# Optimization experiments

Hardware: AMD Instinct MI355X
Metric: run time of the kernel (lower is better)

Reference implementation:

```python
import math
import jax, jax.numpy as jnp
import numpy as np

IMAGE_SIZE = 224


def _resize_bilinear(img, out_h, out_w):
    """PyTorch F.interpolate(mode='bilinear', align_corners=False) equivalent.
    img: [B, H, W] -> [B, out_h, out_w]. No antialiasing (matches torch default)."""
    B, H, W = img.shape

    def coords(out, size):
        r = jnp.maximum((jnp.arange(out, dtype=jnp.float32) + 0.5) * (size / out) - 0.5, 0.0)
        i0 = jnp.minimum(jnp.floor(r).astype(jnp.int32), size - 1)
        i1 = jnp.minimum(i0 + 1, size - 1)
        w = r - i0.astype(jnp.float32)
        return i0, i1, w

    r0, r1, wr = coords(out_h, H)
    c0, c1, wc = coords(out_w, W)
    rows = img[:, r0, :] * (1.0 - wr)[None, :, None] + img[:, r1, :] * wr[None, :, None]
    out = rows[:, :, c0] * (1.0 - wc)[None, None, :] + rows[:, :, c1] * wc[None, None, :]
    return out


def _normalize_minmax(x, eps=1e-8):
    mn = x.min()
    mx = x.max()
    return jnp.where(mx - mn < eps, jnp.zeros_like(x), (x - mn) / (mx - mn + eps))


def _grid_embed(vals, n):
    """Row-major scatter of vals[:, :n] into a ceil(sqrt(n))^2 grid (zero padded)."""
    B = vals.shape[0]
    gs = int(math.ceil(math.sqrt(n)))
    pad = gs * gs - n
    return jnp.pad(vals, ((0, 0), (0, pad))).reshape(B, gs, gs)


def setup_inputs() -> dict:
    key = jax.random.key(0)
    hidden_state = jax.random.normal(key, (32, 512, 4096, 1), dtype=jnp.float32)
    return {"hidden_state": hidden_state}


def reference(hidden_state):
    B, E, N, _ = hidden_state.shape
    x = hidden_state[..., 0]  # [B, E, N]

    # temporal view: mean over nodes -> [B, E] -> grid -> resize
    t_grid = _grid_embed(x.mean(axis=2), E)
    temporal = _normalize_minmax(_resize_bilinear(t_grid, IMAGE_SIZE, IMAGE_SIZE))

    # spatial view: mean over embedding dim -> [B, N] -> grid -> resize
    s_grid = _grid_embed(x.mean(axis=1), N)
    spatial = _normalize_minmax(_resize_bilinear(s_grid, IMAGE_SIZE, IMAGE_SIZE))

    # correlation view: row-normalized centered features, [B, E, E] correlation
    xc = x - x.mean(axis=2, keepdims=True)
    xn = xc / (jnp.linalg.norm(xc, axis=2, keepdims=True) + 1e-8)
    corr = jnp.einsum('bin,bjn->bij', xn, xn)  # [B, E, E]
    correlation = _normalize_minmax(_resize_bilinear(corr, IMAGE_SIZE, IMAGE_SIZE))

    # [B, 3, image_size, image_size]
    return jnp.stack([temporal, spatial, correlation], axis=1)
```

## Files before the change

### kernel.cpp

```cpp
#include <hip/hip_runtime.h>
#include <hip/hip_bf16.h>
#include <math.h>

#define IMG 224
#define PIX (IMG*IMG)
#define B_ 32
#define E_ 512
#define N_ 4096
#define SV_BLOCKS 256
#define SC_ ((float)(512.0/224.0))
#define RPB 16
#define NCHUNK 32
#define KSPLIT 2
#define KLEN (N_/KSPLIT)
#define NTILE 10

typedef __attribute__((ext_vector_type(8))) short bf16x8;
typedef __attribute__((ext_vector_type(4))) float f32x4;

__device__ inline unsigned short f2bf(float f){
  unsigned u = __float_as_uint(f);
  unsigned r = (u + 0x7FFFu + ((u >> 16) & 1u)) >> 16;
  return (unsigned short)r;
}

__global__ void __launch_bounds__(256) stats_y(const float* __restrict__ x,
                                               float* __restrict__ meanv,
                                               float* __restrict__ colpart,
                                               ushort* __restrict__ y){
  int b = blockIdx.x >> 5, chunk = blockIdx.x & 31;
  int e0 = chunk << 4;
  int t = threadIdx.x;
  __shared__ short sInv[512];
  __shared__ float sW[224];
  __shared__ float red[2][16];
  sInv[t] = -1; sInv[t + 256] = -1;
  __syncthreads();
  if (t < 224){
    float r = fmaxf(((float)t + 0.5f) * SC_ - 0.5f, 0.f);
    int r0 = min((int)r, E_ - 1);
    sW[t] = r - (float)r0;
    sInv[r0] = (short)t;
  }
  __syncthreads();

  float cur[16], prev[16], nxt[16], csum[16];
  #pragma unroll
  for (int j = 0; j < 16; j++){ csum[j] = 0.f; prev[j] = 0.f; }
  const float4* row0 = (const float4*)(x + ((size_t)b * E_ + e0) * N_);
  #pragma unroll
  for (int k = 0; k < 4; k++) *(float4*)(cur + 4 * k) = row0[t + 256 * k];
  float pmu = 0.f, prn = 0.f;

  for (int idx = 0; idx <= RPB; idx++){
    int e = e0 + idx;
    if (e >= E_) break;
    bool hasNext = (idx < RPB) && (e + 1 < E_);
    if (hasNext){
      const float4* nr = (const float4*)(x + ((size_t)b * E_ + e + 1) * N_);
      #pragma unroll
      for (int k = 0; k < 4; k++) *(float4*)(nxt + 4 * k) = nr[t + 256 * k];
    }
    float s = 0.f, ss = 0.f;
    #pragma unroll
    for (int j = 0; j < 16; j++){ s += cur[j]; ss += cur[j] * cur[j]; }
    #pragma unroll
    for (int o = 32; o; o >>= 1){ s += __shfl_down(s, o); ss += __shfl_down(ss, o); }
    int wv = t >> 6, ln = t & 63, p = idx & 1;
    if (ln == 0){ red[p][wv] = s; red[p][8 + wv] = ss; }
    __syncthreads();
    float S  = red[p][0] + red[p][1] + red[p][2] + red[p][3];
    float SS = red[p][8] + red[p][9] + red[p][10] + red[p][11];
    float mu = S * (1.f / N_);
    float var = fmaxf(SS - S * S * (1.f / N_), 0.f);
    float rn = 1.f / (sqrtf(var) + 1e-8f);
    if (idx < RPB){
      #pragma unroll
      for (int j = 0; j < 16; j++) csum[j] += cur[j];
      if (t == 0) meanv[b * E_ + e] = mu;
    }
    if (idx >= 1){
      int i = sInv[e - 1];
      if (i >= 0){
        float w = sW[i];
        float a0 = (1.f - w) * prn, a1 = w * rn;
        float cc = -(a0 * pmu + a1 * mu);
        ushort* yo = y + ((size_t)b * IMG + i) * N_;
        #pragma unroll
        for (int k = 0; k < 4; k++){
          union { ushort u[4]; int2 v; } pk;
          #pragma unroll
          for (int j = 0; j < 4; j++)
            pk.u[j] = f2bf(a0 * prev[4*k+j] + a1 * cur[4*k+j] + cc);
          *(int2*)(yo + 1024 * k + 4 * t) = pk.v;
        }
      }
    }
    pmu = mu; prn = rn;
    #pragma unroll
    for (int j = 0; j < 16; j++){ prev[j] = cur[j]; if (hasNext) cur[j] = nxt[j]; }
  }
  float* cp = colpart + ((size_t)(b * NCHUNK + chunk)) * N_;
  #pragma unroll
  for (int k = 0; k < 4; k++) *(float4*)(cp + 1024 * k + 4 * t) = *(float4*)(csum + 4 * k);
}

__global__ void __launch_bounds__(256) col_finalize(const float* __restrict__ colpart,
                                                    float* __restrict__ colmean){
  int b = blockIdx.x >> 4;
  int n = ((blockIdx.x & 15) << 8) + threadIdx.x;
  float s = 0.f;
  #pragma unroll
  for (int c = 0; c < NCHUNK; c++) s += colpart[((size_t)(b * NCHUNK + c)) * N_ + n];
  colmean[b * N_ + n] = s * (1.f / E_);
}

__device__ inline float grid_val(const float* v, int gs, int n, int r, int c){
  int idx = r * gs + c;
  return (idx < n) ? v[idx] : 0.f;
}
__device__ inline float bilin(const float* v, int gs, int n, int i, int j){
  float sc = (float)((double)gs / 224.0);
  float r = fmaxf(((float)i + 0.5f) * sc - 0.5f, 0.f);
  float c = fmaxf(((float)j + 0.5f) * sc - 0.5f, 0.f);
  int r0 = min((int)r, gs - 1), c0 = min((int)c, gs - 1);
  int r1 = min(r0 + 1, gs - 1), c1 = min(c0 + 1, gs - 1);
  float wr = r - (float)r0, wc = c - (float)c0;
  float v00 = grid_val(v, gs, n, r0, c0), v10 = grid_val(v, gs, n, r1, c0);
  float v01 = grid_val(v, gs, n, r0, c1), v11 = grid_val(v, gs, n, r1, c1);
  float ra = v00 * (1.f - wr) + v10 * wr;
  float rb = v01 * (1.f - wr) + v11 * wr;
  return ra * (1.f - wc) + rb * wc;
}

__global__ void __launch_bounds__(256) sv_minmax(const float* __restrict__ meanv,
                                                 const float* __restrict__ colmean,
                                                 float* __restrict__ scr){
  float tmn = INFINITY, tmx = -INFINITY, smn = INFINITY, smx = -INFINITY;
  for (int g = blockIdx.x * 256 + threadIdx.x; g < B_ * PIX; g += SV_BLOCKS * 256){
    int b = g / PIX, p = g - b * PIX;
    int i = p / IMG, j = p - i * IMG;
    float tv = bilin(meanv   + b * E_, 23, E_, i, j);
    float sv = bilin(colmean + b * N_, 64, N_, i, j);
    tmn = fminf(tmn, tv); tmx = fmaxf(tmx, tv);
    smn = fminf(smn, sv); smx = fmaxf(smx, sv);
  }
  #pragma unroll
  for (int o = 32; o; o >>= 1){
    tmn = fminf(tmn, __shfl_down(tmn, o)); tmx = fmaxf(tmx, __shfl_down(tmx, o));
    smn = fminf(smn, __shfl_down(smn, o)); smx = fmaxf(smx, __shfl_down(smx, o));
  }
  __shared__ float red[4][4];
  int wv = threadIdx.x >> 6, ln = threadIdx.x & 63;
  if (ln == 0){ red[wv][0] = tmn; red[wv][1] = tmx; red[wv][2] = smn; red[wv][3] = smx; }
  __syncthreads();
  if (threadIdx.x == 0){
    scr[blockIdx.x * 4 + 0] = fminf(fminf(red[0][0], red[1][0]), fminf(red[2][0], red[3][0]));
    scr[blockIdx.x * 4 + 1] = fmaxf(fmaxf(red[0][1], red[1][1]), fmaxf(red[2][1], red[3][1]));
    scr[blockIdx.x * 4 + 2] = fminf(fminf(red[0][2], red[1][2]), fminf(red[2][2], red[3][2]));
    scr[blockIdx.x * 4 + 3] = fmaxf(fmaxf(red[0][3], red[1][3]), fmaxf(red[2][3], red[3][3]));
  }
}

#define LDSTR 72
__device__ const int TI_[NTILE] = {0,0,0,0,1,1,1,2,2,3};
__device__ const int TJ_[NTILE] = {0,1,2,3,1,2,3,2,3,3};

__global__ void __launch_bounds__(256) corr_gemm_sk(const ushort* __restrict__ y,
                                                    float* __restrict__ partials){
  int xcd  = blockIdx.x & 7;
  int slot = blockIdx.x >> 3;
  int b    = (xcd << 2) + (slot / 20);
  int rem  = slot % 20;
  int ks   = rem / 10;
  int tile = rem - ks * 10;
  int bt   = b * NTILE + tile;
  int ti = TI_[tile], tj = TJ_[tile];
  const ushort* yb = y + (size_t)b * IMG * N_ + (size_t)ks * KLEN;
  __shared__ ushort lA[64 * LDSTR];
  __shared__ ushort lB[64 * LDSTR];
  int t = threadIdx.x;
  int wv = t >> 6, ln = t & 63;
  int wm = wv & 1, wn = wv >> 1;
  int quad = ln >> 4, l16 = ln & 15;
  f32x4 acc[2][2] = {};
  int s = t & 7, r2 = t >> 3;
  int rA0 = min(ti * 64 + r2,      223), rA1 = min(ti * 64 + r2 + 32, 223);
  int rB0 = min(tj * 64 + r2,      223), rB1 = min(tj * 64 + r2 + 32, 223);
  for (int k0 = 0; k0 < KLEN; k0 += 64){
    int4 a0 = *(const int4*)(yb + (size_t)rA0 * N_ + k0 + s * 8);
    int4 a1 = *(const int4*)(yb + (size_t)rA1 * N_ + k0 + s * 8);
    int4 b0v = *(const int4*)(yb + (size_t)rB0 * N_ + k0 + s * 8);
    int4 b1v = *(const int4*)(yb + (size_t)rB1 * N_ + k0 + s * 8);
    __syncthreads();
    *(int4*)(lA + r2 * LDSTR + s * 8)        = a0;
    *(int4*)(lA + (r2 + 32) * LDSTR + s * 8) = a1;
    *(int4*)(lB + r2 * LDSTR + s * 8)        = b0v;
    *(int4*)(lB + (r2 + 32) * LDSTR + s * 8) = b1v;
    __syncthreads();
    #pragma unroll
    for (int kk = 0; kk < 2; kk++){
      bf16x8 af0 = *(const bf16x8*)(lA + (wm * 32 + l16)      * LDSTR + kk * 32 + quad * 8);
      bf16x8 af1 = *(const bf16x8*)(lA + (wm * 32 + 16 + l16) * LDSTR + kk * 32 + quad * 8);
      bf16x8 bf0 = *(const bf16x8*)(lB + (wn * 32 + l16)      * LDSTR + kk * 32 + quad * 8);
      bf16x8 bf1 = *(const bf16x8*)(lB + (wn * 32 + 16 + l16) * LDSTR + kk * 32 + quad * 8);
      acc[0][0] = __builtin_amdgcn_mfma_f32_16x16x32_bf16(af0, bf0, acc[0][0], 0, 0, 0);
      acc[0][1] = __builtin_amdgcn_mfma_f32_16x16x32_bf16(af0, bf1, acc[0][1], 0, 0, 0);
      acc[1][0] = __builtin_amdgcn_mfma_f32_16x16x32_bf16(af1, bf0, acc[1][0], 0, 0, 0);
      acc[1][1] = __builtin_amdgcn_mfma_f32_16x16x32_bf16(af1, bf1, acc[1][1], 0, 0, 0);
    }
  }
  float* pp = partials + ((size_t)ks * (B_ * NTILE) + bt) * 4096 + t * 16;
  #pragma unroll
  for (int im = 0; im < 2; im++)
    #pragma unroll
    for (int in = 0; in < 2; in++)
      *(f32x4*)(pp + 4 * (im * 2 + in)) = acc[im][in];
}

__global__ void __launch_bounds__(256) corr_reduce(const float* __restrict__ partials,
                                                   float* __restrict__ out,
                                                   float* __restrict__ scr){
  int bt = blockIdx.x;
  int b = bt / NTILE, tile = bt - b * NTILE;
  int ti = TI_[tile], tj = TJ_[tile];
  bool diag = (ti == tj);
  int t = threadIdx.x;
  int wv = t >> 6, ln = t & 63;
  int wm = wv & 1, wn = wv >> 1;
  int quad = ln >> 4, l16 = ln & 15;
  f32x4 acc[2][2];
  #pragma unroll
  for (int im = 0; im < 2; im++)
    #pragma unroll
    for (int in = 0; in < 2; in++){
      f32x4 a = {0.f, 0.f, 0.f, 0.f};
      #pragma unroll
      for (int ks = 0; ks < KSPLIT; ks++)
        a += *(const f32x4*)(partials + ((size_t)ks * (B_ * NTILE) + bt) * 4096
                             + t * 16 + 4 * (im * 2 + in));
      acc[im][in] = a;
    }
  float mn = INFINITY, mx = -INFINITY;
  float* ov = out + ((size_t)b * 3 + 2) * PIX;
  #pragma unroll
  for (int im = 0; im < 2; im++)
    #pragma unroll
    for (int in = 0; in < 2; in++){
      int gi0 = ti * 64 + wm * 32 + im * 16 + quad * 4;
      int gj  = tj * 64 + wn * 32 + in * 16 + l16;
      #pragma unroll
      for (int rg = 0; rg < 4; rg++){
        int gi = gi0 + rg;
        if (gi < IMG && gj < IMG){
          float v = acc[im][in][rg];
          ov[gi * IMG + gj] = v;
          mn = fminf(mn, v); mx = fmaxf(mx, v);
        }
      }
      if (!diag && gj < IMG && gi0 < IMG){
        float4 tv;
        tv.x = acc[im][in][0]; tv.y = acc[im][in][1];
        tv.z = acc[im][in][2]; tv.w = acc[im][in][3];
        *(float4*)(ov + gj * IMG + gi0) = tv;
      }
    }
  #pragma unroll
  for (int o = 32; o; o >>= 1){
    mn = fminf(mn, __shfl_down(mn, o)); mx = fmaxf(mx, __shfl_down(mx, o));
  }
  __shared__ float red[4][2];
  if (ln == 0){ red[wv][0] = mn; red[wv][1] = mx; }
  __syncthreads();
  if (t == 0){
    scr[bt * 2 + 0] = fminf(fminf(red[0][0], red[1][0]), fminf(red[2][0], red[3][0]));
    scr[bt * 2 + 1] = fmaxf(fmaxf(red[0][1], red[1][1]), fmaxf(red[2][1], red[3][1]));
  }
}

__global__ void __launch_bounds__(256) reduce_slots(const float* __restrict__ sv_scr,
                                                    const float* __restrict__ corr_scr,
                                                    float* __restrict__ slots){
  int t = threadIdx.x;
  float tmn = sv_scr[4*t+0], tmx = sv_scr[4*t+1];
  float smn = sv_scr[4*t+2], smx = sv_scr[4*t+3];
  float cmn = INFINITY, cmx = -INFINITY;
  for (int idx = t; idx < B_ * NTILE; idx += 256){
    cmn = fminf(cmn, corr_scr[2*idx]);
    cmx = fmaxf(cmx, corr_scr[2*idx+1]);
  }
  #pragma unroll
  for (int o = 32; o; o >>= 1){
    tmn = fminf(tmn, __shfl_down(tmn, o)); tmx = fmaxf(tmx, __shfl_down(tmx, o));
    smn = fminf(smn, __shfl_down(smn, o)); smx = fmaxf(smx, __shfl_down(smx, o));
    cmn = fminf(cmn, __shfl_down(cmn, o)); cmx = fmaxf(cmx, __shfl_down(cmx, o));
  }
  __shared__ float red[4][6];
  int wv = t >> 6, ln = t & 63;
  if (ln == 0){
    red[wv][0]=tmn; red[wv][1]=tmx; red[wv][2]=smn;
    red[wv][3]=smx; red[wv][4]=cmn; red[wv][5]=cmx;
  }
  __syncthreads();
  if (t == 0){
    slots[0] = fminf(fminf(red[0][0],red[1][0]), fminf(red[2][0],red[3][0]));
    slots[1] = fmaxf(fmaxf(red[0][1],red[1][1]), fmaxf(red[2][1],red[3][1]));
    slots[2] = fminf(fminf(red[0][2],red[1][2]), fminf(red[2][2],red[3][2]));
    slots[3] = fmaxf(fmaxf(red[0][3],red[1][3]), fmaxf(red[2][3],red[3][3]));
    slots[4] = fminf(fminf(red[0][4],red[1][4]), fminf(red[2][4],red[3][4]));
    slots[5] = fmaxf(fmaxf(red[0][5],red[1][5]), fmaxf(red[2][5],red[3][5]));
  }
}

__global__ void __launch_bounds__(256) final_write(const float* __restrict__ meanv,
                                                   const float* __restrict__ colmean,
                                                   float* __restrict__ out,
                                                   const float* __restrict__ slots){
  int g = blockIdx.x * 256 + threadIdx.x;
  float tmn = slots[0], tmx = slots[1];
  float smn = slots[2], smx = slots[3];
  int b = g / PIX, p = g - b * PIX;
  int i = p / IMG, j = p - i * IMG;
  float tv = bilin(meanv   + b * E_, 23, E_, i, j);
  float sv = bilin(colmean + b * N_, 64, N_, i, j);
  float td = tmx - tmn, sd = smx - smn;
  out[((size_t)b * 3 + 0) * PIX + p] = (td < 1e-8f) ? 0.f : (tv - tmn) / (td + 1e-8f);
  out[((size_t)b * 3 + 1) * PIX + p] = (sd < 1e-8f) ? 0.f : (sv - smn) / (sd + 1e-8f);
  if (g < B_ * PIX / 4){
    float cmn = slots[4], cmx = slots[5];
    float cd = cmx - cmn;
    float inv = 1.f / (cd + 1e-8f);
    bool z = cd < 1e-8f;
    int c = g * 4;
    int bb = c / PIX, pp = c - bb * PIX;
    float* oc = out + ((size_t)bb * 3 + 2) * PIX + pp;
    float4 v = *(float4*)oc;
    v.x = z ? 0.f : (v.x - cmn) * inv;
    v.y = z ? 0.f : (v.y - cmn) * inv;
    v.z = z ? 0.f : (v.z - cmn) * inv;
    v.w = z ? 0.f : (v.w - cmn) * inv;
    *(float4*)oc = v;
  }
}

extern "C" void kernel_launch(void* const* d_in, const int* in_sizes, int n_in,
                              void* d_out, int out_size, void* d_ws, size_t ws_size,
                              hipStream_t stream){
  const float* x = (const float*)d_in[0];
  float* out = (float*)d_out;
  char* ws = (char*)d_ws;
  float* slots    = (float*)(ws + 0);
  float* meanv    = (float*)(ws + 256);
  float* colmean  = meanv + B_ * E_;
  float* colpart  = colmean + B_ * N_;
  float* sv_scr   = colpart + (size_t)B_ * NCHUNK * N_;
  float* corr_scr = sv_scr + SV_BLOCKS * 4;
  size_t y_off = ((size_t)((char*)(corr_scr + B_ * NTILE * 2) - ws) + 255) & ~(size_t)255;
  ushort* y = (ushort*)(ws + y_off);
  size_t p_off = (y_off + (size_t)B_ * IMG * N_ * 2 + 255) & ~(size_t)255;
  float* partials = (float*)(ws + p_off);

  hipLaunchKernelGGL(stats_y, dim3(B_ * NCHUNK), dim3(256), 0, stream,
                     x, meanv, colpart, y);
  hipLaunchKernelGGL(corr_gemm_sk, dim3(KSPLIT * B_ * NTILE), dim3(256), 0, stream,
                     y, partials);
  hipLaunchKernelGGL(corr_reduce, dim3(B_ * NTILE), dim3(256), 0, stream,
                     partials, out, corr_scr);
  hipLaunchKernelGGL(col_finalize, dim3(B_ * 16), dim3(256), 0, stream,
                     colpart, colmean);
  hipLaunchKernelGGL(sv_minmax, dim3(SV_BLOCKS), dim3(256), 0, stream,
                     meanv, colmean, sv_scr);
  hipLaunchKernelGGL(reduce_slots, dim3(1), dim3(256), 0, stream,
                     sv_scr, corr_scr, slots);
  hipLaunchKernelGGL(final_write, dim3(B_ * PIX / 256), dim3(256), 0, stream,
                     meanv, colmean, out, slots);
}
```

Baseline: 445.3 us.

## Merge small kernels into horizontally fused launches to cut launch count

Cuts the launch chain from seven kernels to four. Column finalization now runs as extra blocks inside the GEMM launch. The correlation reduce and spatial/temporal min-max run as block ranges of one launch. Each final_write block redoes the global slot reduction instead of using a separate single-block kernel. This removes launch overhead and serial gaps between tiny kernels, at the cost of redundant per-block slot reduction work and mixed block types sharing resources.

```diff
diff --git a/kernel.cpp b/kernel.cpp
--- a/kernel.cpp
+++ b/kernel.cpp
@@ -7,13 +7,13 @@
 #define B_ 32
 #define E_ 512
 #define N_ 4096
-#define SV_BLOCKS 256
 #define SC_ ((float)(512.0/224.0))
 #define RPB 16
 #define NCHUNK 32
 #define KSPLIT 2
 #define KLEN (N_/KSPLIT)
 #define NTILE 10
+#define LDSTR 72
 
 typedef __attribute__((ext_vector_type(8))) short bf16x8;
 typedef __attribute__((ext_vector_type(4))) float f32x4;
@@ -105,16 +105,6 @@
   for (int k = 0; k < 4; k++) *(float4*)(cp + 1024 * k + 4 * t) = *(float4*)(csum + 4 * k);
 }
 
-__global__ void __launch_bounds__(256) col_finalize(const float* __restrict__ colpart,
-                                                    float* __restrict__ colmean){
-  int b = blockIdx.x >> 4;
-  int n = ((blockIdx.x & 15) << 8) + threadIdx.x;
-  float s = 0.f;
-  #pragma unroll
-  for (int c = 0; c < NCHUNK; c++) s += colpart[((size_t)(b * NCHUNK + c)) * N_ + n];
-  colmean[b * N_ + n] = s * (1.f / E_);
-}
-
 __device__ inline float grid_val(const float* v, int gs, int n, int r, int c){
   int idx = r * gs + c;
   return (idx < n) ? v[idx] : 0.f;
@@ -133,43 +123,28 @@
   return ra * (1.f - wc) + rb * wc;
 }
 
-__global__ void __launch_bounds__(256) sv_minmax(const float* __restrict__ meanv,
-                                                 const float* __restrict__ colmean,
-                                                 float* __restrict__ scr){
-  float tmn = INFINITY, tmx = -INFINITY, smn = INFINITY, smx = -INFINITY;
-  for (int g = blockIdx.x * 256 + threadIdx.x; g < B_ * PIX; g += SV_BLOCKS * 256){
-    int b = g / PIX, p = g - b * PIX;
-    int i = p / IMG, j = p - i * IMG;
-    float tv = bilin(meanv   + b * E_, 23, E_, i, j);
-    float sv = bilin(colmean + b * N_, 64, N_, i, j);
-    tmn = fminf(tmn, tv); tmx = fmaxf(tmx, tv);
-    smn = fminf(smn, sv); smx = fmaxf(smx, sv);
-  }
-  #pragma unroll
-  for (int o = 32; o; o >>= 1){
-    tmn = fminf(tmn, __shfl_down(tmn, o)); tmx = fmaxf(tmx, __shfl_down(tmx, o));
-    smn = fminf(smn, __shfl_down(smn, o)); smx = fmaxf(smx, __shfl_down(smx, o));
-  }
-  __shared__ float red[4][4];
-  int wv = threadIdx.x >> 6, ln = threadIdx.x & 63;
-  if (ln == 0){ red[wv][0] = tmn; red[wv][1] = tmx; red[wv][2] = smn; red[wv][3] = smx; }
-  __syncthreads();
-  if (threadIdx.x == 0){
-    scr[blockIdx.x * 4 + 0] = fminf(fminf(red[0][0], red[1][0]), fminf(red[2][0], red[3][0]));
-    scr[blockIdx.x * 4 + 1] = fmaxf(fmaxf(red[0][1], red[1][1]), fmaxf(red[2][1], red[3][1]));
-    scr[blockIdx.x * 4 + 2] = fminf(fminf(red[0][2], red[1][2]), fminf(red[2][2], red[3][2]));
-    scr[blockIdx.x * 4 + 3] = fmaxf(fmaxf(red[0][3], red[1][3]), fmaxf(red[2][3], red[3][3]));
-  }
-}
-
-#define LDSTR 72
 __device__ const int TI_[NTILE] = {0,0,0,0,1,1,1,2,2,3};
 __device__ const int TJ_[NTILE] = {0,1,2,3,1,2,3,2,3,3};
 
-__global__ void __launch_bounds__(256) corr_gemm_sk(const ushort* __restrict__ y,
-                                                    float* __restrict__ partials){
-  int xcd  = blockIdx.x & 7;
-  int slot = blockIdx.x >> 3;
+__global__ void __launch_bounds__(256) gemm_colfin(const ushort* __restrict__ y,
+                                                   float* __restrict__ partials,
+                                                   const float* __restrict__ colpart,
+                                                   float* __restrict__ colmean){
+  int bid = blockIdx.x;
+  int t = threadIdx.x;
+  if (bid >= 640){
+    for (int u = bid - 640; u < 512; u += 128){
+      int b = u >> 4;
+      int n = ((u & 15) << 8) + t;
+      float s = 0.f;
+      #pragma unroll
+      for (int c = 0; c < NCHUNK; c++) s += colpart[((size_t)(b * NCHUNK + c)) * N_ + n];
+      colmean[b * N_ + n] = s * (1.f / E_);
+    }
+    return;
+  }
+  int xcd  = bid & 7;
+  int slot = bid >> 3;
   int b    = (xcd << 2) + (slot / 20);
   int rem  = slot % 20;
   int ks   = rem / 10;
@@ -179,7 +154,6 @@
   const ushort* yb = y + (size_t)b * IMG * N_ + (size_t)ks * KLEN;
   __shared__ ushort lA[64 * LDSTR];
   __shared__ ushort lB[64 * LDSTR];
-  int t = threadIdx.x;
   int wv = t >> 6, ln = t & 63;
   int wm = wv & 1, wn = wv >> 1;
   int quad = ln >> 4, l16 = ln & 15;
@@ -218,107 +192,139 @@
       *(f32x4*)(pp + 4 * (im * 2 + in)) = acc[im][in];
 }
 
-__global__ void __launch_bounds__(256) corr_reduce(const float* __restrict__ partials,
-                                                   float* __restrict__ out,
-                                                   float* __restrict__ scr){
-  int bt = blockIdx.x;
-  int b = bt / NTILE, tile = bt - b * NTILE;
-  int ti = TI_[tile], tj = TJ_[tile];
-  bool diag = (ti == tj);
+__global__ void __launch_bounds__(256) reduce_sv(const float* __restrict__ partials,
+                                                 const float* __restrict__ meanv,
+                                                 const float* __restrict__ colmean,
+                                                 float* __restrict__ out,
+                                                 float* __restrict__ corr_scr,
+                                                 float* __restrict__ sv_scr){
+  int bid = blockIdx.x;
   int t = threadIdx.x;
   int wv = t >> 6, ln = t & 63;
-  int wm = wv & 1, wn = wv >> 1;
-  int quad = ln >> 4, l16 = ln & 15;
-  f32x4 acc[2][2];
-  #pragma unroll
-  for (int im = 0; im < 2; im++)
-    #pragma unroll
-    for (int in = 0; in < 2; in++){
-      f32x4 a = {0.f, 0.f, 0.f, 0.f};
-      #pragma unroll
-      for (int ks = 0; ks < KSPLIT; ks++)
-        a += *(const f32x4*)(partials + ((size_t)ks * (B_ * NTILE) + bt) * 4096
-                             + t * 16 + 4 * (im * 2 + in));
-      acc[im][in] = a;
-    }
-  float mn = INFINITY, mx = -INFINITY;
-  float* ov = out + ((size_t)b * 3 + 2) * PIX;
-  #pragma unroll
-  for (int im = 0; im < 2; im++)
-    #pragma unroll
-    for (int in = 0; in < 2; in++){
-      int gi0 = ti * 64 + wm * 32 + im * 16 + quad * 4;
-      int gj  = tj * 64 + wn * 32 + in * 16 + l16;
-      #pragma unroll
-      for (int rg = 0; rg < 4; rg++){
-        int gi = gi0 + rg;
-        if (gi < IMG && gj < IMG){
-          float v = acc[im][in][rg];
-          ov[gi * IMG + gj] = v;
-          mn = fminf(mn, v); mx = fmaxf(mx, v);
+  __shared__ float red[4][4];
+  if (bid < B_ * NTILE){
+    int bt = bid;
+    int b = bt / NTILE, tile = bt - b * NTILE;
+    int ti = TI_[tile], tj = TJ_[tile];
+    bool diag = (ti == tj);
+    int wm = wv & 1, wn = wv >> 1;
+    int quad = ln >> 4, l16 = ln & 15;
+    f32x4 acc[2][2];
+    #pragma unroll
+    for (int im = 0; im < 2; im++)
+      #pragma unroll
+      for (int in = 0; in < 2; in++){
+        f32x4 a = {0.f, 0.f, 0.f, 0.f};
+        #pragma unroll
+        for (int ks = 0; ks < KSPLIT; ks++)
+          a += *(const f32x4*)(partials + ((size_t)ks * (B_ * NTILE) + bt) * 4096
+                               + t * 16 + 4 * (im * 2 + in));
+        acc[im][in] = a;
+      }
+    float mn = INFINITY, mx = -INFINITY;
+    float* ov = out + ((size_t)b * 3 + 2) * PIX;
+    #pragma unroll
+    for (int im = 0; im < 2; im++)
+      #pragma unroll
+      for (int in = 0; in < 2; in++){
+        int gi0 = ti * 64 + wm * 32 + im * 16 + quad * 4;
+        int gj  = tj * 64 + wn * 32 + in * 16 + l16;
+        #pragma unroll
+        for (int rg = 0; rg < 4; rg++){
+          int gi = gi0 + rg;
+          if (gi < IMG && gj < IMG){
+            float v = acc[im][in][rg];
+            ov[gi * IMG + gj] = v;
+            mn = fminf(mn, v); mx = fmaxf(mx, v);
+          }
+        }
+        if (!diag && gj < IMG && gi0 < IMG){
+          float4 tv;
+          tv.x = acc[im][in][0]; tv.y = acc[im][in][1];
+          tv.z = acc[im][in][2]; tv.w = acc[im][in][3];
+          *(float4*)(ov + gj * IMG + gi0) = tv;
         }
       }
-      if (!diag && gj < IMG && gi0 < IMG){
-        float4 tv;
-        tv.x = acc[im][in][0]; tv.y = acc[im][in][1];
-        tv.z = acc[im][in][2]; tv.w = acc[im][in][3];
-        *(float4*)(ov + gj * IMG + gi0) = tv;
-      }
-    }
-  #pragma unroll
-  for (int o = 32; o; o >>= 1){
-    mn = fminf(mn, __shfl_down(mn, o)); mx = fmaxf(mx, __shfl_down(mx, o));
-  }
-  __shared__ float red[4][2];
-  if (ln == 0){ red[wv][0] = mn; red[wv][1] = mx; }
-  __syncthreads();
-  if (t == 0){
-    scr[bt * 2 + 0] = fminf(fminf(red[0][0], red[1][0]), fminf(red[2][0], red[3][0]));
-    scr[bt * 2 + 1] = fmaxf(fmaxf(red[0][1], red[1][1]), fmaxf(red[2][1], red[3][1]));
-  }
-}
-
-__global__ void __launch_bounds__(256) reduce_slots(const float* __restrict__ sv_scr,
-                                                    const float* __restrict__ corr_scr,
-                                                    float* __restrict__ slots){
-  int t = threadIdx.x;
-  float tmn = sv_scr[4*t+0], tmx = sv_scr[4*t+1];
-  float smn = sv_scr[4*t+2], smx = sv_scr[4*t+3];
-  float cmn = INFINITY, cmx = -INFINITY;
-  for (int idx = t; idx < B_ * NTILE; idx += 256){
-    cmn = fminf(cmn, corr_scr[2*idx]);
-    cmx = fmaxf(cmx, corr_scr[2*idx+1]);
-  }
-  #pragma unroll
-  for (int o = 32; o; o >>= 1){
-    tmn = fminf(tmn, __shfl_down(tmn, o)); tmx = fmaxf(tmx, __shfl_down(tmx, o));
-    smn = fminf(smn, __shfl_down(smn, o)); smx = fmaxf(smx, __shfl_down(smx, o));
-    cmn = fminf(cmn, __shfl_down(cmn, o)); cmx = fmaxf(cmx, __shfl_down(cmx, o));
-  }
-  __shared__ float red[4][6];
-  int wv = t >> 6, ln = t & 63;
-  if (ln == 0){
-    red[wv][0]=tmn; red[wv][1]=tmx; red[wv][2]=smn;
-    red[wv][3]=smx; red[wv][4]=cmn; red[wv][5]=cmx;
-  }
-  __syncthreads();
-  if (t == 0){
-    slots[0] = fminf(fminf(red[0][0],red[1][0]), fminf(red[2][0],red[3][0]));
-    slots[1] = fmaxf(fmaxf(red[0][1],red[1][1]), fmaxf(red[2][1],red[3][1]));
-    slots[2] = fminf(fminf(red[0][2],red[1][2]), fminf(red[2][2],red[3][2]));
-    slots[3] = fmaxf(fmaxf(red[0][3],red[1][3]), fmaxf(red[2][3],red[3][3]));
-    slots[4] = fminf(fminf(red[0][4],red[1][4]), fminf(red[2][4],red[3][4]));
-    slots[5] = fmaxf(fmaxf(red[0][5],red[1][5]), fmaxf(red[2][5],red[3][5]));
+    #pragma unroll
+    for (int o = 32; o; o >>= 1){
+      mn = fminf(mn, __shfl_down(mn, o)); mx = fmaxf(mx, __shfl_down(mx, o));
+    }
+    if (ln == 0){ red[wv][0] = mn; red[wv][1] = mx; }
+    __syncthreads();
+    if (t == 0){
+      corr_scr[bt * 2 + 0] = fminf(fminf(red[0][0], red[1][0]), fminf(red[2][0], red[3][0]));
+      corr_scr[bt * 2 + 1] = fmaxf(fmaxf(red[0][1], red[1][1]), fmaxf(red[2][1], red[3][1]));
+    }
+  } else {
+    int vb = bid - B_ * NTILE;
+    float tmn = INFINITY, tmx = -INFINITY, smn = INFINITY, smx = -INFINITY;
+    for (int g = vb * 256 + t; g < B_ * PIX; g += 256 * 256){
+      int b = g / PIX, p = g - b * PIX;
+      int i = p / IMG, j = p - i * IMG;
+      float tv = bilin(meanv   + b * E_, 23, E_, i, j);
+      float sv = bilin(colmean + b * N_, 64, N_, i, j);
+      tmn = fminf(tmn, tv); tmx = fmaxf(tmx, tv);
+      smn = fminf(smn, sv); smx = fmaxf(smx, sv);
+    }
+    #pragma unroll
+    for (int o = 32; o; o >>= 1){
+      tmn = fminf(tmn, __shfl_down(tmn, o)); tmx = fmaxf(tmx, __shfl_down(tmx, o));
+      smn = fminf(smn, __shfl_down(smn, o)); smx = fmaxf(smx, __shfl_down(smx, o));
+    }
+    if (ln == 0){ red[wv][0] = tmn; red[wv][1] = tmx; red[wv][2] = smn; red[wv][3] = smx; }
+    __syncthreads();
+    if (t == 0){
+      sv_scr[vb * 4 + 0] = fminf(fminf(red[0][0], red[1][0]), fminf(red[2][0], red[3][0]));
+      sv_scr[vb * 4 + 1] = fmaxf(fmaxf(red[0][1], red[1][1]), fmaxf(red[2][1], red[3][1]));
+      sv_scr[vb * 4 + 2] = fminf(fminf(red[0][2], red[1][2]), fminf(red[2][2], red[3][2]));
+      sv_scr[vb * 4 + 3] = fmaxf(fmaxf(red[0][3], red[1][3]), fmaxf(red[2][3], red[3][3]));
+    }
   }
 }
 
 __global__ void __launch_bounds__(256) final_write(const float* __restrict__ meanv,
                                                    const float* __restrict__ colmean,
                                                    float* __restrict__ out,
-                                                   const float* __restrict__ slots){
-  int g = blockIdx.x * 256 + threadIdx.x;
-  float tmn = slots[0], tmx = slots[1];
-  float smn = slots[2], smx = slots[3];
+                                                   const float* __restrict__ sv_scr,
+                                                   const float* __restrict__ corr_scr){
+  int t = threadIdx.x;
+  int wv = t >> 6, ln = t & 63;
+  __shared__ float red6[4][6];
+  __shared__ float slot6[6];
+  {
+    float tmn = sv_scr[4*t+0], tmx = sv_scr[4*t+1];
+    float smn = sv_scr[4*t+2], smx = sv_scr[4*t+3];
+    float cmn = INFINITY, cmx = -INFINITY;
+    for (int idx = t; idx < B_ * NTILE; idx += 256){
+      cmn = fminf(cmn, corr_scr[2*idx]);
+      cmx = fmaxf(cmx, corr_scr[2*idx+1]);
+    }
+    #pragma unroll
+    for (int o = 32; o; o >>= 1){
+      tmn = fminf(tmn, __shfl_down(tmn, o)); tmx = fmaxf(tmx, __shfl_down(tmx, o));
+      smn = fminf(smn, __shfl_down(smn, o)); smx = fmaxf(smx, __shfl_down(smx, o));
+      cmn = fminf(cmn, __shfl_down(cmn, o)); cmx = fmaxf(cmx, __shfl_down(cmx, o));
+    }
+    if (ln == 0){
+      red6[wv][0]=tmn; red6[wv][1]=tmx; red6[wv][2]=smn;
+      red6[wv][3]=smx; red6[wv][4]=cmn; red6[wv][5]=cmx;
+    }
+    __syncthreads();
+    if (t == 0){
+      slot6[0] = fminf(fminf(red6[0][0],red6[1][0]), fminf(red6[2][0],red6[3][0]));
+      slot6[1] = fmaxf(fmaxf(red6[0][1],red6[1][1]), fmaxf(red6[2][1],red6[3][1]));
+      slot6[2] = fminf(fminf(red6[0][2],red6[1][2]), fminf(red6[2][2],red6[3][2]));
+      slot6[3] = fmaxf(fmaxf(red6[0][3],red6[1][3]), fmaxf(red6[2][3],red6[3][3]));
+      slot6[4] = fminf(fminf(red6[0][4],red6[1][4]), fminf(red6[2][4],red6[3][4]));
+      slot6[5] = fmaxf(fmaxf(red6[0][5],red6[1][5]), fmaxf(red6[2][5],red6[3][5]));
+    }
+    __syncthreads();
+  }
+  float tmn = slot6[0], tmx = slot6[1];
+  float smn = slot6[2], smx = slot6[3];
+  float cmn = slot6[4], cmx = slot6[5];
+
+  int g = blockIdx.x * 256 + t;
   int b = g / PIX, p = g - b * PIX;
   int i = p / IMG, j = p - i * IMG;
   float tv = bilin(meanv   + b * E_, 23, E_, i, j);
@@ -327,7 +333,6 @@
   out[((size_t)b * 3 + 0) * PIX + p] = (td < 1e-8f) ? 0.f : (tv - tmn) / (td + 1e-8f);
   out[((size_t)b * 3 + 1) * PIX + p] = (sd < 1e-8f) ? 0.f : (sv - smn) / (sd + 1e-8f);
   if (g < B_ * PIX / 4){
-    float cmn = slots[4], cmx = slots[5];
     float cd = cmx - cmn;
     float inv = 1.f / (cd + 1e-8f);
     bool z = cd < 1e-8f;
@@ -349,12 +354,11 @@
   const float* x = (const float*)d_in[0];
   float* out = (float*)d_out;
   char* ws = (char*)d_ws;
-  float* slots    = (float*)(ws + 0);
   float* meanv    = (float*)(ws + 256);
   float* colmean  = meanv + B_ * E_;
   float* colpart  = colmean + B_ * N_;
   float* sv_scr   = colpart + (size_t)B_ * NCHUNK * N_;
-  float* corr_scr = sv_scr + SV_BLOCKS * 4;
+  float* corr_scr = sv_scr + 256 * 4;
   size_t y_off = ((size_t)((char*)(corr_scr + B_ * NTILE * 2) - ws) + 255) & ~(size_t)255;
   ushort* y = (ushort*)(ws + y_off);
   size_t p_off = (y_off + (size_t)B_ * IMG * N_ * 2 + 255) & ~(size_t)255;
@@ -362,16 +366,10 @@
 
   hipLaunchKernelGGL(stats_y, dim3(B_ * NCHUNK), dim3(256), 0, stream,
                      x, meanv, colpart, y);
-  hipLaunchKernelGGL(corr_gemm_sk, dim3(KSPLIT * B_ * NTILE), dim3(256), 0, stream,
-                     y, partials);
-  hipLaunchKernelGGL(corr_reduce, dim3(B_ * NTILE), dim3(256), 0, stream,
-                     partials, out, corr_scr);
-  hipLaunchKernelGGL(col_finalize, dim3(B_ * 16), dim3(256), 0, stream,
-                     colpart, colmean);
-  hipLaunchKernelGGL(sv_minmax, dim3(SV_BLOCKS), dim3(256), 0, stream,
-                     meanv, colmean, sv_scr);
-  hipLaunchKernelGGL(reduce_slots, dim3(1), dim3(256), 0, stream,
-                     sv_scr, corr_scr, slots);
+  hipLaunchKernelGGL(gemm_colfin, dim3(768), dim3(256), 0, stream,
+                     y, partials, colpart, colmean);
+  hipLaunchKernelGGL(reduce_sv, dim3(B_ * NTILE + 256), dim3(256), 0, stream,
+                     partials, meanv, colmean, out, corr_scr, sv_scr);
   hipLaunchKernelGGL(final_write, dim3(B_ * PIX / 256), dim3(256), 0, stream,
-                     meanv, colmean, out, slots);
-}
+                     meanv, colmean, out, sv_scr, corr_scr);
+}
```

Result: no change. 444.4 us (-0.2%).
